# Optimization experiments

Hardware: AMD Instinct MI355X
Metric: run time of the kernel (lower is better)

The kernel has to match this reference:

```python
import jax, jax.numpy as jnp
import numpy as np

B, D, LC, LQ = 16, 512, 2048, 512
NEG_INF = -1e30


def setup_inputs() -> dict:
    key = jax.random.key(0)
    k1, k2, k3 = jax.random.split(key, 3)
    C = jax.random.normal(k1, (B, D, LC), dtype=jnp.float32)
    Q = jax.random.normal(k2, (B, D, LQ), dtype=jnp.float32)
    cmask = jnp.ones((B, LC), dtype=bool)
    qmask = jnp.ones((B, LQ), dtype=bool)
    lim = np.sqrt(1.0 / D)
    w = jax.random.uniform(k3, (3 * D,), dtype=jnp.float32, minval=-lim, maxval=lim)
    return {"C": C, "Q": Q, "cmask": cmask, "qmask": qmask, "w": w}


def reference(C, Q, cmask, qmask, w):
    d = C.shape[1]
    Cb = jnp.swapaxes(C, 1, 2)  # (B, Lc, d)
    Qb = jnp.swapaxes(Q, 1, 2)  # (B, Lq, d)
    w1, w2, w3 = w[:d], w[d:2 * d], w[2 * d:]
    # Trilinear similarity, decomposed: S[b,i,j] = C_i.w1 + Q_j.w2 + (C_i*w3).Q_j
    S = (Cb @ w1)[:, :, None] + (Qb @ w2)[:, None, :] \
        + jnp.einsum('bid,bjd->bij', Cb * w3, Qb)  # (B, Lc, Lq)
    S1 = jax.nn.softmax(jnp.where(qmask[:, None, :], S, NEG_INF), axis=2)
    S2 = jax.nn.softmax(jnp.where(cmask[:, :, None], S, NEG_INF), axis=1)
    A = S1 @ Qb                                     # (B, Lc, d)
    Bt = (S1 @ jnp.swapaxes(S2, 1, 2)) @ Cb         # (B, Lc, d)
    out = jnp.concatenate([Cb, A, Cb * A, Cb * Bt], axis=2)  # (B, Lc, 4d)
    return jnp.swapaxes(out, 1, 2)  # (B, 4d, Lc); dropout inactive at inference
```

## Files before the change

### kernel.cpp

```cpp
#include <hip/hip_runtime.h>
#include <stdint.h>

#define Bn 16
#define Dn 512
#define LCn 2048
#define LQn 512

typedef __attribute__((ext_vector_type(8))) short s8v;
typedef __attribute__((ext_vector_type(4))) short s4v;
typedef __attribute__((ext_vector_type(4))) float f4v;

__device__ __forceinline__ unsigned short f2bf(float f) {
  union { float f; uint32_t u; } v; v.f = f;
  uint32_t r = v.u + 0x7FFFu + ((v.u >> 16) & 1u);
  return (unsigned short)(r >> 16);
}

__device__ __forceinline__ void async16(void* lds, const void* g) {
  __builtin_amdgcn_global_load_lds((const __attribute__((address_space(1))) void*)g,
                                   (__attribute__((address_space(3))) void*)lds, 16, 0, 0);
}

#define WAITVM(N) asm volatile("s_waitcnt vmcnt(" #N ")")
#define WAITLGKM0 asm volatile("s_waitcnt lgkmcnt(0)")

typedef __attribute__((address_space(3))) const unsigned short* lds_csp;
__device__ __forceinline__ s8v ldsr(const unsigned short* p) {
  s8v r;
  asm volatile("ds_read_b128 %0, %1" : "=v"(r) : "v"((lds_csp)p));
  return r;
}


template <int KSTEPS>
__device__ __forceinline__ void gemm_core(const unsigned short* __restrict__ Ag,
                                          const unsigned short* __restrict__ Bg,
                                          int lda, int ldb,
                                          unsigned short* As, unsigned short* Bs,
                                          f4v acc[4][4]) {
  const int t = threadIdx.x;
  const int lane = t & 63, quad = lane >> 4, l16 = lane & 15;
  const int wm = (t >> 6) & 1, wn = t >> 7;
  const int rowA = t >> 2;
  const int koff = (t & 3) << 3;
  const unsigned short* ga0 = Ag + (size_t)rowA * lda + koff;
  const unsigned short* ga1 = Ag + (size_t)(rowA + 64) * lda + koff;
  const unsigned short* gb0 = Bg + (size_t)rowA * ldb + koff;
  const unsigned short* gb1 = Bg + (size_t)(rowA + 64) * ldb + koff;
  auto stage = [&](int buf, int k) {
    async16(As + buf + t * 8, ga0 + k);
    async16(As + buf + (t + 256) * 8, ga1 + k);
    async16(Bs + buf + t * 8, gb0 + k);
    async16(Bs + buf + (t + 256) * 8, gb1 + k);
  };
  stage(0, 0);
  stage(4096, 32);
  for (int ks = 0; ks < KSTEPS; ++ks) {
    const int cur = (ks & 1) ? 4096 : 0;
    if (ks < KSTEPS - 1) { WAITVM(4); } else { WAITVM(0); }
    __builtin_amdgcn_s_barrier();
    __builtin_amdgcn_sched_barrier(0);
    s8v af[4], bf[4];
#pragma unroll
    for (int mt = 0; mt < 4; ++mt)
      af[mt] = ldsr(As + cur + (wm * 64 + mt * 16 + l16) * 32 + quad * 8);
#pragma unroll
    for (int nt = 0; nt < 4; ++nt)
      bf[nt] = ldsr(Bs + cur + (wn * 64 + nt * 16 + l16) * 32 + quad * 8);
    WAITLGKM0;
    __builtin_amdgcn_sched_barrier(0);
    __builtin_amdgcn_s_barrier();
    __builtin_amdgcn_sched_barrier(0);
    if (ks + 2 < KSTEPS) stage(cur, (ks + 2) << 5);
    __builtin_amdgcn_s_setprio(1);
#pragma unroll
    for (int mt = 0; mt < 4; ++mt)
#pragma unroll
      for (int nt = 0; nt < 4; ++nt)
        acc[mt][nt] = __builtin_amdgcn_mfma_f32_16x16x32_bf16(af[mt], bf[nt], acc[mt][nt], 0, 0, 0);
    __builtin_amdgcn_s_setprio(0);
  }
}

template <int KSTEPS>
__device__ __forceinline__ void gemm_core2(const unsigned short* __restrict__ Ag,
                                           const unsigned short* __restrict__ Bg0,
                                           const unsigned short* __restrict__ Bg1,
                                           int lda, int ldb,
                                           unsigned short* As, unsigned short* Bs0,
                                           unsigned short* Bs1,
                                           f4v accA[4][4], f4v accB[4][4]) {
  const int t = threadIdx.x;
  const int lane = t & 63, quad = lane >> 4, l16 = lane & 15;
  const int wm = (t >> 6) & 1, wn = t >> 7;
  const int rowA = t >> 2;
  const int koff = (t & 3) << 3;
  const unsigned short* ga0 = Ag + (size_t)rowA * lda + koff;
  const unsigned short* ga1 = Ag + (size_t)(rowA + 64) * lda + koff;
  const unsigned short* gq0 = Bg0 + (size_t)rowA * ldb + koff;
  const unsigned short* gq1 = Bg0 + (size_t)(rowA + 64) * ldb + koff;
  const unsigned short* gt0 = Bg1 + (size_t)rowA * ldb + koff;
  const unsigned short* gt1 = Bg1 + (size_t)(rowA + 64) * ldb + koff;
  auto stage = [&](int buf, int k) {
    async16(As + buf + t * 8, ga0 + k);
    async16(As + buf + (t + 256) * 8, ga1 + k);
    async16(Bs0 + buf + t * 8, gq0 + k);
    async16(Bs0 + buf + (t + 256) * 8, gq1 + k);
    async16(Bs1 + buf + t * 8, gt0 + k);
    async16(Bs1 + buf + (t + 256) * 8, gt1 + k);
  };
  stage(0, 0);
  stage(4096, 32);
  for (int ks = 0; ks < KSTEPS; ++ks) {
    const int cur = (ks & 1) ? 4096 : 0;
    if (ks < KSTEPS - 1) { WAITVM(6); } else { WAITVM(0); }
    __builtin_amdgcn_s_barrier();
    __builtin_amdgcn_sched_barrier(0);
    s8v af[4], bq[4], bt[4];
#pragma unroll
    for (int mt = 0; mt < 4; ++mt)
      af[mt] = ldsr(As + cur + (wm * 64 + mt * 16 + l16) * 32 + quad * 8);
#pragma unroll
    for (int nt = 0; nt < 4; ++nt) {
      bq[nt] = ldsr(Bs0 + cur + (wn * 64 + nt * 16 + l16) * 32 + quad * 8);
      bt[nt] = ldsr(Bs1 + cur + (wn * 64 + nt * 16 + l16) * 32 + quad * 8);
    }
    WAITLGKM0;
    __builtin_amdgcn_sched_barrier(0);
    __builtin_amdgcn_s_barrier();
    __builtin_amdgcn_sched_barrier(0);
    if (ks + 2 < KSTEPS) stage(cur, (ks + 2) << 5);
    __builtin_amdgcn_s_setprio(1);
#pragma unroll
    for (int mt = 0; mt < 4; ++mt)
#pragma unroll
      for (int nt = 0; nt < 4; ++nt) {
        accA[mt][nt] = __builtin_amdgcn_mfma_f32_16x16x32_bf16(af[mt], bq[nt], accA[mt][nt], 0, 0, 0);
        accB[mt][nt] = __builtin_amdgcn_mfma_f32_16x16x32_bf16(af[mt], bt[nt], accB[mt][nt], 0, 0, 0);
      }
    __builtin_amdgcn_s_setprio(0);
  }
}

template <int KSTEPS>
__device__ __forceinline__ void gemm_coreT(const unsigned short* __restrict__ Ag,
                                           const unsigned short* __restrict__ Bg,
                                           int lda, int ldb,
                                           unsigned short* As, unsigned short* Bs,
                                           f4v acc[4][2]) {
  const int t = threadIdx.x;
  const int lane = t & 63, quad = lane >> 4, l16 = lane & 15;
  const int wave = t >> 6, wm = wave & 1, wn = wave >> 1;
  const int rowA = t >> 2;
  const int koff = (t & 3) << 3;
  const unsigned short* ga = Ag + (size_t)rowA * lda + koff;
  const unsigned short* gb = Bg + (size_t)rowA * ldb + koff;
  auto stage = [&](int buf, int k) {
    async16(As + buf + t * 8, ga + k);
    async16(Bs + buf + t * 8, gb + k);
  };
  stage(0, 0);
  stage(4096, 32);
  for (int ks = 0; ks < KSTEPS; ++ks) {
    const int cur = (ks & 1) ? 4096 : 0;
    if (ks < KSTEPS - 1) { WAITVM(2); } else { WAITVM(0); }
    __builtin_amdgcn_s_barrier();
    __builtin_amdgcn_sched_barrier(0);
    s8v af[4], bf[2];
#pragma unroll
    for (int mt = 0; mt < 4; ++mt)
      af[mt] = ldsr(As + cur + (wm * 64 + mt * 16 + l16) * 32 + quad * 8);
#pragma unroll
    for (int nt = 0; nt < 2; ++nt)
      bf[nt] = ldsr(Bs + cur + (wn * 32 + nt * 16 + l16) * 32 + quad * 8);
    WAITLGKM0;
    __builtin_amdgcn_sched_barrier(0);
    __builtin_amdgcn_s_barrier();
    __builtin_amdgcn_sched_barrier(0);
    if (ks + 2 < KSTEPS) stage(cur, (ks + 2) << 5);
    __builtin_amdgcn_s_setprio(1);
#pragma unroll
    for (int mt = 0; mt < 4; ++mt)
#pragma unroll
      for (int nt = 0; nt < 2; ++nt)
        acc[mt][nt] = __builtin_amdgcn_mfma_f32_16x16x32_bf16(af[mt], bf[nt], acc[mt][nt], 0, 0, 0);
    __builtin_amdgcn_s_setprio(0);
  }
}

#define EPILOGUE_IDS                                              \
  const int t = threadIdx.x, lane = t & 63, quad = lane >> 4,     \
            l16 = lane & 15;                                      \
  const int wave = t >> 6, wm = wave & 1, wn = wave >> 1;         \
  (void)lane;

#define ACC_ZERO(acc)                                             \
  _Pragma("unroll") for (int _i = 0; _i < 4; ++_i)                \
  _Pragma("unroll") for (int _j = 0; _j < 4; ++_j)                \
      acc[_i][_j] = (f4v){0.f, 0.f, 0.f, 0.f};


__global__ __launch_bounds__(256) void k_castC(const float* __restrict__ C,
                                               const float* __restrict__ w,
                                               unsigned short* __restrict__ Cbf,
                                               unsigned short* __restrict__ Ct,
                                               float* __restrict__ cw) {
  __shared__ unsigned short tile[64][66];
  __shared__ float red[4][64];
  const int b = blockIdx.z, i0 = blockIdx.x * 64, d0 = blockIdx.y * 64;
  const int t = threadIdx.x, il = t & 63, dq = t >> 6;
  float part = 0.f;
#pragma unroll 4
  for (int r = 0; r < 16; ++r) {
    const int dl = r * 4 + dq;
    const size_t gi = ((size_t)b * Dn + d0 + dl) * LCn + i0 + il;
    const float v = C[gi];
    const unsigned short h = f2bf(v);
    Cbf[gi] = h;
    tile[dl][il] = h;
    part += v * w[d0 + dl];
  }
  red[dq][il] = part;
  __syncthreads();
  if (t < 64) {
    atomicAdd(&cw[b * LCn + i0 + t], red[0][t] + red[1][t] + red[2][t] + red[3][t]);
  }
#pragma unroll 4
  for (int r = 0; r < 16; ++r) {
    const int i_l = r * 4 + dq;
    Ct[((size_t)b * LCn + i0 + i_l) * Dn + d0 + il] = tile[il][i_l];
  }
}

__global__ __launch_bounds__(256) void k_castQ(const float* __restrict__ Q,
                                               const float* __restrict__ w,
                                               unsigned short* __restrict__ Qbf,
                                               unsigned short* __restrict__ Q3t,
                                               float* __restrict__ qw) {
  __shared__ unsigned short tile[64][66];
  __shared__ float red[4][64];
  const int b = blockIdx.z, j0 = blockIdx.x * 64, d0 = blockIdx.y * 64;
  const int t = threadIdx.x, jl = t & 63, dq = t >> 6;
  float part = 0.f;
#pragma unroll 4
  for (int r = 0; r < 16; ++r) {
    const int dl = r * 4 + dq;
    const size_t gi = ((size_t)b * Dn + d0 + dl) * LQn + j0 + jl;
    const float v = Q[gi];
    Qbf[gi] = f2bf(v);
    tile[dl][jl] = f2bf(v * w[2 * Dn + d0 + dl]);
    part += v * w[Dn + d0 + dl];
  }
  red[dq][jl] = part;
  __syncthreads();
  if (t < 64) {
    atomicAdd(&qw[b * LQn + j0 + t], red[0][t] + red[1][t] + red[2][t] + red[3][t]);
  }
#pragma unroll 4
  for (int r = 0; r < 16; ++r) {
    const int j_l = r * 4 + dq;
    Q3t[((size_t)b * LQn + j0 + j_l) * Dn + d0 + jl] = tile[jl][j_l];
  }
}


union SmU {
  struct { unsigned short A[8192]; unsigned short B[8192]; } st;
  unsigned short e[4][64 * 72];
};

__global__ __launch_bounds__(256) void k_gemm1(
    const unsigned short* __restrict__ Ct, const unsigned short* __restrict__ Q3t,
    const float* __restrict__ cw, const float* __restrict__ qw,
    unsigned short* __restrict__ E, unsigned short* __restrict__ ET,
    float* __restrict__ srow, float* __restrict__ scol) {
  __shared__ __align__(16) SmU sm;
  const int b = blockIdx.z, m0 = blockIdx.x * 128, n0 = blockIdx.y * 128;
  const unsigned short* Ag = Ct + ((size_t)b * LCn + m0) * Dn;
  const unsigned short* Bg = Q3t + ((size_t)b * LQn + n0) * Dn;
  f4v acc[4][4];
  ACC_ZERO(acc)
  gemm_core<16>(Ag, Bg, Dn, Dn, sm.st.A, sm.st.B, acc);

  EPILOGUE_IDS
  const int R0 = m0 + wm * 64, C0 = n0 + wn * 64;
  float qws[4];
#pragma unroll
  for (int nt = 0; nt < 4; ++nt) qws[nt] = qw[b * LQn + C0 + nt * 16 + l16];
#pragma unroll
  for (int mt = 0; mt < 4; ++mt) {
    const f4v cw4 = *(const f4v*)(cw + b * LCn + R0 + mt * 16 + quad * 4);
#pragma unroll
    for (int nt = 0; nt < 4; ++nt)
#pragma unroll
      for (int r = 0; r < 4; ++r)
        acc[mt][nt][r] = __expf(acc[mt][nt][r] + cw4[r] + qws[nt]);
  }
#pragma unroll
  for (int mt = 0; mt < 4; ++mt)
#pragma unroll
    for (int r = 0; r < 4; ++r) {
      float v = acc[mt][0][r] + acc[mt][1][r] + acc[mt][2][r] + acc[mt][3][r];
      v += __shfl_xor(v, 1, 64);
      v += __shfl_xor(v, 2, 64);
      v += __shfl_xor(v, 4, 64);
      v += __shfl_xor(v, 8, 64);
      if (l16 == 0) atomicAdd(&srow[b * LCn + R0 + mt * 16 + quad * 4 + r], v);
    }
#pragma unroll
  for (int nt = 0; nt < 4; ++nt) {
    float v = 0.f;
#pragma unroll
    for (int mt = 0; mt < 4; ++mt)
#pragma unroll
      for (int r = 0; r < 4; ++r) v += acc[mt][nt][r];
    v += __shfl_xor(v, 16, 64);
    v += __shfl_xor(v, 32, 64);
    if (quad == 0) atomicAdd(&scol[b * LQn + C0 + nt * 16 + l16], v);
  }
  __syncthreads();
#pragma unroll
  for (int mt = 0; mt < 4; ++mt)
#pragma unroll
    for (int nt = 0; nt < 4; ++nt)
#pragma unroll
      for (int r = 0; r < 4; ++r)
        sm.e[wave][(mt * 16 + quad * 4 + r) * 72 + nt * 16 + l16] = f2bf(acc[mt][nt][r]);
  __syncthreads();
  {
    const int row = t >> 1, half = t & 1;
    const unsigned short* src = sm.e[(row >> 6) | (half << 1)] + (row & 63) * 72;
    unsigned short* dst = E + ((size_t)b * LCn + m0 + row) * LQn + n0 + half * 64;
#pragma unroll
    for (int k = 0; k < 8; ++k) *(s8v*)(dst + k * 8) = *(const s8v*)(src + k * 8);
  }
  {
    const int jrow = t >> 1, ihalf = t & 1;
    const unsigned short* esrc = sm.e[ihalf | ((jrow >> 6) << 1)];
    const int jl = jrow & 63;
    unsigned short* dst = ET + ((size_t)b * LQn + n0 + jrow) * LCn + m0 + ihalf * 64;
#pragma unroll
    for (int k8 = 0; k8 < 8; ++k8) {
      s8v v;
#pragma unroll
      for (int u = 0; u < 8; ++u)
        ((unsigned short*)&v)[u] = esrc[(k8 * 8 + u) * 72 + jl];
      *(s8v*)(dst + k8 * 8) = v;
    }
  }
}

__global__ __launch_bounds__(512) void k_gemmT(
    const unsigned short* __restrict__ ET, const unsigned short* __restrict__ Cbf,
    const float* __restrict__ scol, unsigned short* __restrict__ Tst) {
  __shared__ __align__(16) union {
    struct { unsigned short A[8192]; unsigned short B[8192]; } st;
    unsigned short tt[128][136];
  } sm;
  const int b = blockIdx.z;
  const int m0 = blockIdx.x * 128;
  const int n0 = blockIdx.y * 128;
  const unsigned short* Ag = ET + ((size_t)b * LQn + m0) * LCn;
  const unsigned short* Bg = Cbf + ((size_t)b * Dn + n0) * LCn;
  f4v acc[4][2];
#pragma unroll
  for (int i = 0; i < 4; ++i)
#pragma unroll
    for (int j = 0; j < 2; ++j) acc[i][j] = (f4v){0.f, 0.f, 0.f, 0.f};
  gemm_coreT<64>(Ag, Bg, LCn, LCn, sm.st.A, sm.st.B, acc);

  const int t = threadIdx.x, lane = t & 63, quad = lane >> 4, l16 = lane & 15;
  const int wave = t >> 6, wm = wave & 1, wn = wave >> 1;
  (void)lane;
  __syncthreads();
#pragma unroll
  for (int mt = 0; mt < 4; ++mt) {
    const int jl = wm * 64 + mt * 16 + quad * 4;
    const f4v sc = *(const f4v*)(scol + b * LQn + m0 + jl);
    f4v inv;
#pragma unroll
    for (int r = 0; r < 4; ++r) inv[r] = 1.0f / sc[r];
#pragma unroll
    for (int nt = 0; nt < 2; ++nt) {
      const int dl = wn * 32 + nt * 16 + l16;
#pragma unroll
      for (int r = 0; r < 4; ++r)
        sm.tt[dl][jl + r] = f2bf(acc[mt][nt][r] * inv[r]);
    }
  }
  __syncthreads();
  {
    const int dl = t >> 2, ch = (t & 3) * 32;
    unsigned short* dst = Tst + ((size_t)b * Dn + n0 + dl) * LQn + m0 + ch;
#pragma unroll
    for (int u = 0; u < 4; ++u)
      *(s8v*)(dst + u * 8) = *(const s8v*)(&sm.tt[dl][ch + u * 8]);
  }
}

__global__ __launch_bounds__(256) void k_gemmAB(
    const unsigned short* __restrict__ E, const unsigned short* __restrict__ Qbf,
    const unsigned short* __restrict__ Tst, const float* __restrict__ srow,
    const float* __restrict__ C, float* __restrict__ out) {
  __shared__ __align__(16) unsigned short As[8192];
  __shared__ __align__(16) unsigned short Bs0[8192];
  __shared__ __align__(16) unsigned short Bs1[8192];
  const int b = blockIdx.z, m0 = blockIdx.x * 128, n0 = blockIdx.y * 128;
  const unsigned short* Ag = E + ((size_t)b * LCn + m0) * LQn;
  const unsigned short* Bg0 = Qbf + ((size_t)b * Dn + n0) * LQn;
  const unsigned short* Bg1 = Tst + ((size_t)b * Dn + n0) * LQn;
  f4v accA[4][4], accB[4][4];
  ACC_ZERO(accA)
  ACC_ZERO(accB)
  gemm_core2<16>(Ag, Bg0, Bg1, LQn, LQn, As, Bs0, Bs1, accA, accB);

  EPILOGUE_IDS
  const int Ri = m0 + wm * 64, Cd = n0 + wn * 64;
#pragma unroll
  for (int mt = 0; mt < 4; ++mt) {
    const int ib = Ri + mt * 16 + quad * 4;
    const f4v sr4 = *(const f4v*)(srow + b * LCn + ib);
    f4v inv;
#pragma unroll
    for (int r = 0; r < 4; ++r) inv[r] = 1.0f / sr4[r];
#pragma unroll
    for (int nt = 0; nt < 4; ++nt) {
      const int d = Cd + nt * 16 + l16;
      const f4v c4 = *(const f4v*)(C + ((size_t)b * Dn + d) * LCn + ib);
      f4v a4, ca, bt4, cb;
#pragma unroll
      for (int r = 0; r < 4; ++r) {
        a4[r] = accA[mt][nt][r] * inv[r];
        ca[r] = c4[r] * a4[r];
        bt4[r] = accB[mt][nt][r] * inv[r];
        cb[r] = c4[r] * bt4[r];
      }
      float* ob = out + (size_t)b * (4 * Dn) * LCn + (size_t)d * LCn + ib;
      *(f4v*)(ob) = c4;
      *(f4v*)(ob + (size_t)Dn * LCn) = a4;
      *(f4v*)(ob + (size_t)(2 * Dn) * LCn) = ca;
      *(f4v*)(ob + (size_t)(3 * Dn) * LCn) = cb;
    }
  }
}

extern "C" void kernel_launch(void* const* d_in, const int* in_sizes, int n_in,
                              void* d_out, int out_size, void* d_ws, size_t ws_size,
                              hipStream_t stream) {
  (void)in_sizes; (void)n_in; (void)out_size; (void)ws_size;
  const float* C = (const float*)d_in[0];
  const float* Q = (const float*)d_in[1];
  const float* w = (const float*)d_in[4];
  float* out = (float*)d_out;

  char* ws = (char*)d_ws;
  size_t off = 0;
  auto alloc = [&](size_t bytes) {
    char* p = ws + off;
    off += (bytes + 255) & ~(size_t)255;
    return p;
  };
  unsigned short* Cbf = (unsigned short*)alloc((size_t)Bn * Dn * LCn * 2);
  unsigned short* Ct  = (unsigned short*)alloc((size_t)Bn * LCn * Dn * 2);
  unsigned short* Qbf = (unsigned short*)alloc((size_t)Bn * Dn * LQn * 2);
  unsigned short* Q3t = (unsigned short*)alloc((size_t)Bn * LQn * Dn * 2);
  unsigned short* E   = (unsigned short*)alloc((size_t)Bn * LCn * LQn * 2);
  unsigned short* ET  = (unsigned short*)alloc((size_t)Bn * LQn * LCn * 2);
  unsigned short* Tst = (unsigned short*)alloc((size_t)Bn * Dn * LQn * 2);
  float* stats = (float*)alloc((size_t)(2 * Bn * LCn + 2 * Bn * LQn) * 4);
  float* cw = stats;
  float* qw = cw + Bn * LCn;
  float* srow = qw + Bn * LQn;
  float* scol = srow + Bn * LCn;

  hipMemsetAsync(stats, 0, (size_t)(2 * Bn * LCn + 2 * Bn * LQn) * 4, stream);
  k_castC<<<dim3(LCn / 64, Dn / 64, Bn), 256, 0, stream>>>(C, w, Cbf, Ct, cw);
  k_castQ<<<dim3(LQn / 64, Dn / 64, Bn), 256, 0, stream>>>(Q, w, Qbf, Q3t, qw);
  k_gemm1<<<dim3(LCn / 128, LQn / 128, Bn), 256, 0, stream>>>(Ct, Q3t, cw, qw, E, ET, srow, scol);
  k_gemmT<<<dim3(LQn / 128, Dn / 128, Bn), 512, 0, stream>>>(ET, Cbf, scol, Tst);
  k_gemmAB<<<dim3(LCn / 128, Dn / 128, Bn), 256, 0, stream>>>(E, Qbf, Tst, srow, C, out);
}
```

Measured before the change: 534.8 us.

## Interleave LDS fragment reads with MFMAs and retile gemmT to 128x64

The three GEMM cores now issue the B-fragment LDS reads in stages. Each MFMA column group starts as soon as its fragments arrive, using partial lgkmcnt waits, and the last group runs after the next global-to-LDS prefetch is issued. This aims to hide LDS read latency behind matrix work instead of waiting for every read before computing. Separately, k_gemmT moves from 512-thread 128x128 tiles to 256-thread 128x64 tiles with a smaller B buffer, which doubles the grid and changes occupancy. The risk is that the epilogue, which is not fully visible, may still assume the old tile shape.

```diff
diff --git a/kernel.cpp b/kernel.cpp
--- a/kernel.cpp
+++ b/kernel.cpp
@@ -22,7 +22,8 @@
 }
 
 #define WAITVM(N) asm volatile("s_waitcnt vmcnt(" #N ")")
-#define WAITLGKM0 asm volatile("s_waitcnt lgkmcnt(0)")
+#define WAITLGKM(N) asm volatile("s_waitcnt lgkmcnt(" #N ")")
+#define SCHEDBAR __builtin_amdgcn_sched_barrier(0)
 
 typedef __attribute__((address_space(3))) const unsigned short* lds_csp;
 __device__ __forceinline__ s8v ldsr(const unsigned short* p) {
@@ -55,29 +56,44 @@
   };
   stage(0, 0);
   stage(4096, 32);
+  const unsigned short* Aw = As + (wm * 64 + l16) * 32 + quad * 8;
+  const unsigned short* Bw = Bs + (wn * 64 + l16) * 32 + quad * 8;
   for (int ks = 0; ks < KSTEPS; ++ks) {
     const int cur = (ks & 1) ? 4096 : 0;
     if (ks < KSTEPS - 1) { WAITVM(4); } else { WAITVM(0); }
     __builtin_amdgcn_s_barrier();
-    __builtin_amdgcn_sched_barrier(0);
+    SCHEDBAR;
     s8v af[4], bf[4];
 #pragma unroll
-    for (int mt = 0; mt < 4; ++mt)
-      af[mt] = ldsr(As + cur + (wm * 64 + mt * 16 + l16) * 32 + quad * 8);
-#pragma unroll
-    for (int nt = 0; nt < 4; ++nt)
-      bf[nt] = ldsr(Bs + cur + (wn * 64 + nt * 16 + l16) * 32 + quad * 8);
-    WAITLGKM0;
-    __builtin_amdgcn_sched_barrier(0);
+    for (int mt = 0; mt < 4; ++mt) af[mt] = ldsr(Aw + cur + mt * 512);
+    bf[0] = ldsr(Bw + cur);
+    bf[1] = ldsr(Bw + cur + 512);
+    WAITLGKM(1);
+    SCHEDBAR;
+    __builtin_amdgcn_s_setprio(1);
+    bf[2] = ldsr(Bw + cur + 1024);
+#pragma unroll
+    for (int mt = 0; mt < 4; ++mt)
+      acc[mt][0] = __builtin_amdgcn_mfma_f32_16x16x32_bf16(af[mt], bf[0], acc[mt][0], 0, 0, 0);
+    WAITLGKM(1);
+    SCHEDBAR;
+    bf[3] = ldsr(Bw + cur + 1536);
+#pragma unroll
+    for (int mt = 0; mt < 4; ++mt)
+      acc[mt][1] = __builtin_amdgcn_mfma_f32_16x16x32_bf16(af[mt], bf[1], acc[mt][1], 0, 0, 0);
+    WAITLGKM(1);
+    SCHEDBAR;
+#pragma unroll
+    for (int mt = 0; mt < 4; ++mt)
+      acc[mt][2] = __builtin_amdgcn_mfma_f32_16x16x32_bf16(af[mt], bf[2], acc[mt][2], 0, 0, 0);
+    WAITLGKM(0);
+    SCHEDBAR;
     __builtin_amdgcn_s_barrier();
-    __builtin_amdgcn_sched_barrier(0);
+    SCHEDBAR;
     if (ks + 2 < KSTEPS) stage(cur, (ks + 2) << 5);
-    __builtin_amdgcn_s_setprio(1);
-#pragma unroll
-    for (int mt = 0; mt < 4; ++mt)
-#pragma unroll
-      for (int nt = 0; nt < 4; ++nt)
-        acc[mt][nt] = __builtin_amdgcn_mfma_f32_16x16x32_bf16(af[mt], bf[nt], acc[mt][nt], 0, 0, 0);
+#pragma unroll
+    for (int mt = 0; mt < 4; ++mt)
+      acc[mt][3] = __builtin_amdgcn_mfma_f32_16x16x32_bf16(af[mt], bf[3], acc[mt][3], 0, 0, 0);
     __builtin_amdgcn_s_setprio(0);
   }
 }
@@ -111,33 +127,53 @@
   };
   stage(0, 0);
   stage(4096, 32);
+  const unsigned short* Aw = As + (wm * 64 + l16) * 32 + quad * 8;
+  const unsigned short* Qw = Bs0 + (wn * 64 + l16) * 32 + quad * 8;
+  const unsigned short* Tw = Bs1 + (wn * 64 + l16) * 32 + quad * 8;
   for (int ks = 0; ks < KSTEPS; ++ks) {
     const int cur = (ks & 1) ? 4096 : 0;
     if (ks < KSTEPS - 1) { WAITVM(6); } else { WAITVM(0); }
     __builtin_amdgcn_s_barrier();
-    __builtin_amdgcn_sched_barrier(0);
+    SCHEDBAR;
     s8v af[4], bq[4], bt[4];
 #pragma unroll
-    for (int mt = 0; mt < 4; ++mt)
-      af[mt] = ldsr(As + cur + (wm * 64 + mt * 16 + l16) * 32 + quad * 8);
-#pragma unroll
-    for (int nt = 0; nt < 4; ++nt) {
-      bq[nt] = ldsr(Bs0 + cur + (wn * 64 + nt * 16 + l16) * 32 + quad * 8);
-      bt[nt] = ldsr(Bs1 + cur + (wn * 64 + nt * 16 + l16) * 32 + quad * 8);
-    }
-    WAITLGKM0;
-    __builtin_amdgcn_sched_barrier(0);
+    for (int mt = 0; mt < 4; ++mt) af[mt] = ldsr(Aw + cur + mt * 512);
+    bq[0] = ldsr(Qw + cur);       bt[0] = ldsr(Tw + cur);
+    bq[1] = ldsr(Qw + cur + 512); bt[1] = ldsr(Tw + cur + 512);
+    WAITLGKM(2);
+    SCHEDBAR;
+    __builtin_amdgcn_s_setprio(1);
+    bq[2] = ldsr(Qw + cur + 1024); bt[2] = ldsr(Tw + cur + 1024);
+#pragma unroll
+    for (int mt = 0; mt < 4; ++mt) {
+      accA[mt][0] = __builtin_amdgcn_mfma_f32_16x16x32_bf16(af[mt], bq[0], accA[mt][0], 0, 0, 0);
+      accB[mt][0] = __builtin_amdgcn_mfma_f32_16x16x32_bf16(af[mt], bt[0], accB[mt][0], 0, 0, 0);
+    }
+    WAITLGKM(2);
+    SCHEDBAR;
+    bq[3] = ldsr(Qw + cur + 1536); bt[3] = ldsr(Tw + cur + 1536);
+#pragma unroll
+    for (int mt = 0; mt < 4; ++mt) {
+      accA[mt][1] = __builtin_amdgcn_mfma_f32_16x16x32_bf16(af[mt], bq[1], accA[mt][1], 0, 0, 0);
+      accB[mt][1] = __builtin_amdgcn_mfma_f32_16x16x32_bf16(af[mt], bt[1], accB[mt][1], 0, 0, 0);
+    }
+    WAITLGKM(2);
+    SCHEDBAR;
+#pragma unroll
+    for (int mt = 0; mt < 4; ++mt) {
+      accA[mt][2] = __builtin_amdgcn_mfma_f32_16x16x32_bf16(af[mt], bq[2], accA[mt][2], 0, 0, 0);
+      accB[mt][2] = __builtin_amdgcn_mfma_f32_16x16x32_bf16(af[mt], bt[2], accB[mt][2], 0, 0, 0);
+    }
+    WAITLGKM(0);
+    SCHEDBAR;
     __builtin_amdgcn_s_barrier();
-    __builtin_amdgcn_sched_barrier(0);
+    SCHEDBAR;
     if (ks + 2 < KSTEPS) stage(cur, (ks + 2) << 5);
-    __builtin_amdgcn_s_setprio(1);
-#pragma unroll
-    for (int mt = 0; mt < 4; ++mt)
-#pragma unroll
-      for (int nt = 0; nt < 4; ++nt) {
-        accA[mt][nt] = __builtin_amdgcn_mfma_f32_16x16x32_bf16(af[mt], bq[nt], accA[mt][nt], 0, 0, 0);
-        accB[mt][nt] = __builtin_amdgcn_mfma_f32_16x16x32_bf16(af[mt], bt[nt], accB[mt][nt], 0, 0, 0);
-      }
+#pragma unroll
+    for (int mt = 0; mt < 4; ++mt) {
+      accA[mt][3] = __builtin_amdgcn_mfma_f32_16x16x32_bf16(af[mt], bq[3], accA[mt][3], 0, 0, 0);
+      accB[mt][3] = __builtin_amdgcn_mfma_f32_16x16x32_bf16(af[mt], bt[3], accB[mt][3], 0, 0, 0);
+    }
     __builtin_amdgcn_s_setprio(0);
   }
 }
@@ -150,40 +186,46 @@
                                            f4v acc[4][2]) {
   const int t = threadIdx.x;
   const int lane = t & 63, quad = lane >> 4, l16 = lane & 15;
-  const int wave = t >> 6, wm = wave & 1, wn = wave >> 1;
+  const int wm = (t >> 6) & 1, wn = t >> 7;
   const int rowA = t >> 2;
   const int koff = (t & 3) << 3;
-  const unsigned short* ga = Ag + (size_t)rowA * lda + koff;
+  const unsigned short* ga0 = Ag + (size_t)rowA * lda + koff;
+  const unsigned short* ga1 = Ag + (size_t)(rowA + 64) * lda + koff;
   const unsigned short* gb = Bg + (size_t)rowA * ldb + koff;
-  auto stage = [&](int buf, int k) {
-    async16(As + buf + t * 8, ga + k);
-    async16(Bs + buf + t * 8, gb + k);
+  auto stage = [&](int abuf, int bbuf, int k) {
+    async16(As + abuf + t * 8, ga0 + k);
+    async16(As + abuf + (t + 256) * 8, ga1 + k);
+    async16(Bs + bbuf + t * 8, gb + k);
   };
-  stage(0, 0);
-  stage(4096, 32);
+  stage(0, 0, 0);
+  stage(4096, 2048, 32);
+  const unsigned short* Aw = As + (wm * 64 + l16) * 32 + quad * 8;
+  const unsigned short* Bw = Bs + (wn * 32 + l16) * 32 + quad * 8;
   for (int ks = 0; ks < KSTEPS; ++ks) {
-    const int cur = (ks & 1) ? 4096 : 0;
-    if (ks < KSTEPS - 1) { WAITVM(2); } else { WAITVM(0); }
+    const int curA = (ks & 1) ? 4096 : 0;
+    const int curB = (ks & 1) ? 2048 : 0;
+    if (ks < KSTEPS - 1) { WAITVM(3); } else { WAITVM(0); }
     __builtin_amdgcn_s_barrier();
-    __builtin_amdgcn_sched_barrier(0);
+    SCHEDBAR;
     s8v af[4], bf[2];
 #pragma unroll
-    for (int mt = 0; mt < 4; ++mt)
-      af[mt] = ldsr(As + cur + (wm * 64 + mt * 16 + l16) * 32 + quad * 8);
-#pragma unroll
-    for (int nt = 0; nt < 2; ++nt)
-      bf[nt] = ldsr(Bs + cur + (wn * 32 + nt * 16 + l16) * 32 + quad * 8);
-    WAITLGKM0;
-    __builtin_amdgcn_sched_barrier(0);
+    for (int mt = 0; mt < 4; ++mt) af[mt] = ldsr(Aw + curA + mt * 512);
+    bf[0] = ldsr(Bw + curB);
+    bf[1] = ldsr(Bw + curB + 512);
+    WAITLGKM(1);
+    SCHEDBAR;
+    __builtin_amdgcn_s_setprio(1);
+#pragma unroll
+    for (int mt = 0; mt < 4; ++mt)
+      acc[mt][0] = __builtin_amdgcn_mfma_f32_16x16x32_bf16(af[mt], bf[0], acc[mt][0], 0, 0, 0);
+    WAITLGKM(0);
+    SCHEDBAR;
     __builtin_amdgcn_s_barrier();
-    __builtin_amdgcn_sched_barrier(0);
-    if (ks + 2 < KSTEPS) stage(cur, (ks + 2) << 5);
-    __builtin_amdgcn_s_setprio(1);
-#pragma unroll
-    for (int mt = 0; mt < 4; ++mt)
-#pragma unroll
-      for (int nt = 0; nt < 2; ++nt)
-        acc[mt][nt] = __builtin_amdgcn_mfma_f32_16x16x32_bf16(af[mt], bf[nt], acc[mt][nt], 0, 0, 0);
+    SCHEDBAR;
+    if (ks + 2 < KSTEPS) stage(curA, curB, (ks + 2) << 5);
+#pragma unroll
+    for (int mt = 0; mt < 4; ++mt)
+      acc[mt][1] = __builtin_amdgcn_mfma_f32_16x16x32_bf16(af[mt], bf[1], acc[mt][1], 0, 0, 0);
     __builtin_amdgcn_s_setprio(0);
   }
 }
@@ -350,16 +392,16 @@
   }
 }
 
-__global__ __launch_bounds__(512) void k_gemmT(
+__global__ __launch_bounds__(256) void k_gemmT(
     const unsigned short* __restrict__ ET, const unsigned short* __restrict__ Cbf,
     const float* __restrict__ scol, unsigned short* __restrict__ Tst) {
   __shared__ __align__(16) union {
-    struct { unsigned short A[8192]; unsigned short B[8192]; } st;
-    unsigned short tt[128][136];
+    struct { unsigned short A[8192]; unsigned short B[4096]; } st;
+    unsigned short tt[64][136];
   } sm;
   const int b = blockIdx.z;
   const int m0 = blockIdx.x * 128;
-  const int n0 = blockIdx.y * 128;
+  const int n0 = blockIdx.y * 64;
   const unsigned short* Ag = ET + ((size_t)b * LQn + m0) * LCn;
   const unsigned short* Bg = Cbf + ((size_t)b * Dn + n0) * LCn;
   f4v acc[4][2];
@@ -477,6 +519,6 @@
   k_castC<<<dim3(LCn / 64, Dn / 64, Bn), 256, 0, stream>>>(C, w, Cbf, Ct, cw);
   k_castQ<<<dim3(LQn / 64, Dn / 64, Bn), 256, 0, stream>>>(Q, w, Qbf, Q3t, qw);
   k_gemm1<<<dim3(LCn / 128, LQn / 128, Bn), 256, 0, stream>>>(Ct, Q3t, cw, qw, E, ET, srow, scol);
-  k_gemmT<<<dim3(LQn / 128, Dn / 128, Bn), 512, 0, stream>>>(ET, Cbf, scol, Tst);
+  k_gemmT<<<dim3(LQn / 128, Dn / 64, Bn), 256, 0, stream>>>(ET, Cbf, scol, Tst);
   k_gemmAB<<<dim3(LCn / 128, Dn / 128, Bn), 256, 0, stream>>>(E, Qbf, Tst, srow, C, out);
 }
```

After: 545.0 us. About the same (+1.9%).
